# Performance work log

Hardware: AMD Instinct MI355X
Metric: run time of the kernel (lower is better)

Reference implementation:

```python
import jax, jax.numpy as jnp
import numpy as np

DIM = 20
N = 200000
E = 6400000
ITERATIONS = 3


def setup_inputs() -> dict:
    key = jax.random.key(0)
    ks = jax.random.split(key, 20)
    inp = {
        "h": jax.random.normal(ks[0], (N, DIM), dtype=jnp.float32),
        "node2depth": jax.random.randint(ks[1], (N,), 0, 5, dtype=jnp.int32),
        "edge_src": jax.random.randint(ks[2], (E,), 0, N, dtype=jnp.int32),
        "edge_dst": jax.random.randint(ks[3], (E,), 0, N, dtype=jnp.int32),
    }
    # Six DIM x DIM Linear layers (weight stored [out,in] like torch, plus bias)
    scale = 1.0 / np.sqrt(DIM)
    names = ["Wz", "Uz", "Wr", "Ur", "Wh", "Uh"]
    for j, nm in enumerate(names):
        inp[nm + "_w"] = jax.random.uniform(ks[4 + 2 * j], (DIM, DIM), jnp.float32, -scale, scale)
        inp[nm + "_b"] = jax.random.uniform(ks[5 + 2 * j], (DIM,), jnp.float32, -scale, scale)
    return inp


def _linear(x, w, b):
    return x @ w.T + b


def reference(h, Wz_w, Wz_b, Uz_w, Uz_b, Wr_w, Wr_b, Ur_w, Ur_b,
              Wh_w, Wh_b, Uh_w, Uh_b, node2depth, edge_src, edge_dst):
    active = None
    for i in range(ITERATIONS):
        # active set shrinks as i grows (depth + i <= ITERATIONS)
        active = (node2depth + i) <= ITERATIONS  # [N] bool
        af = active.astype(h.dtype)
        # x[u] = sum over neighbors v of h[v], counting only active src AND active dst
        msg = h[edge_src] * af[edge_src][:, None]          # [E, DIM]
        x = jax.ops.segment_sum(msg, edge_dst, num_segments=N)  # [N, DIM]
        x = x * af[:, None]
        z = jax.nn.sigmoid(_linear(x, Wz_w, Wz_b) + _linear(h, Uz_w, Uz_b))
        r = jax.nn.sigmoid(_linear(x, Wr_w, Wr_b) + _linear(h, Ur_w, Ur_b))
        h_cand = jnp.tanh(_linear(x, Wh_w, Wh_b) + _linear(r * h, Uh_w, Uh_b))
        h_new = z * h + (1.0 - z) * h_cand
        # inactive nodes are dropped from the dict in the original; since the
        # active set only shrinks, keeping their old h is equivalent
        h = jnp.where(active[:, None], h_new, h)
    # original returns only nodes active at the last iteration; zero out the rest
    return jnp.where(active[:, None], h, jnp.zeros_like(h))
```

## Files before the change

### kernel.cpp

```cpp
#include <hip/hip_runtime.h>

#define DIM    20
#define NN     200000
#define EE     6400000
#define ITERS  3
#define BLOCK  256

#define NODES_PER_FINE   64
#define NFINE            3125
#define NCOARSE          98
#define FINE_PER_COARSE  32

#define TILE1            2048
#define IPT1             8

#define TILE             4096
#define IPT              16

#define CAP1             57344
#define NT2P             14
#define CAP2             2048
#define PQ               2

typedef unsigned int u32;

__global__ void init_cursors(int* __restrict__ coarse_cursor,
                             int* __restrict__ fine_cursor,
                             int* __restrict__ gcur) {
    int g = blockIdx.x * 256 + threadIdx.x;
    if (g < NCOARSE) coarse_cursor[g] = g * CAP1;
    if (g < NFINE)   fine_cursor[g]   = g * CAP2;
    if (g == 0) *gcur = 0;
}

__global__ __launch_bounds__(BLOCK) void kdep(const int* __restrict__ depth,
                                              int* __restrict__ dcnt) {
    __shared__ u32 dh[5];
    int tid = threadIdx.x;
    if (tid < 5) dh[tid] = 0;
    __syncthreads();
    for (int n = blockIdx.x * BLOCK + tid; n < NN; n += gridDim.x * BLOCK)
        atomicAdd(&dh[depth[n]], 1u);
    __syncthreads();
    if (tid < 5) dcnt[tid * 256 + blockIdx.x] = (int)dh[tid];
}

__global__ __launch_bounds__(BLOCK) void k2_scan(const int* __restrict__ dcnt,
                                                 int* __restrict__ dbase,
                                                 int* __restrict__ cum) {
    __shared__ int wsum[4];
    __shared__ int sdb[1281];
    int tid = threadIdx.x;
    int lane = tid & 63, wid = tid >> 6;
    const int CH2 = 5;
    int loc[CH2];
    int base = tid * CH2;
    int s = 0;
    #pragma unroll
    for (int j = 0; j < CH2; ++j) { int v = dcnt[base + j]; loc[j] = v; s += v; }
    int incl = s;
    #pragma unroll
    for (int off = 1; off < 64; off <<= 1) {
        int t = __shfl_up(incl, off, 64);
        if (lane >= off) incl += t;
    }
    if (lane == 63) wsum[wid] = incl;
    __syncthreads();
    int woff = 0;
    for (int w = 0; w < wid; ++w) woff += wsum[w];
    int run = woff + incl - s;
    #pragma unroll
    for (int j = 0; j < CH2; ++j) {
        sdb[base + j]   = run;
        dbase[base + j] = run;
        run += loc[j];
    }
    if (tid == 255) sdb[1280] = run;
    __syncthreads();
    if (tid < 5) cum[tid] = sdb[(tid + 1) * 256];
}

__global__ __launch_bounds__(BLOCK) void kd_scatter(const int* __restrict__ depth,
                                                    const int* __restrict__ dbase,
                                                    int* __restrict__ perm) {
    __shared__ u32 dh[5];
    int tid = threadIdx.x;
    if (tid < 5) dh[tid] = 0;
    __syncthreads();
    for (int n = blockIdx.x * BLOCK + tid; n < NN; n += gridDim.x * BLOCK) {
        int d = depth[n];
        u32 r = atomicAdd(&dh[d], 1u);
        perm[n] = dbase[d * 256 + blockIdx.x] + (int)r;
    }
}

__global__ __launch_bounds__(BLOCK) void p1_split(const int* __restrict__ esrc,
                                                  const int* __restrict__ edst,
                                                  const int* __restrict__ perm,
                                                  const int* __restrict__ cum,
                                                  int* __restrict__ coarse_cursor,
                                                  u32* __restrict__ buf1) {
    __shared__ u32 hist[NCOARSE];
    __shared__ u32 lbase[NCOARSE];
    __shared__ u32 gbase[NCOARSE];
    __shared__ u32 lout[TILE1];
    int tid = threadIdx.x;
    int start = blockIdx.x * TILE1;
    if (tid < NCOARSE) hist[tid] = 0;
    __syncthreads();
    const u32 c3 = (u32)cum[3];

    int4 d4[2], s4[2];
    #pragma unroll
    for (int q = 0; q < 2; ++q) {
        int e4 = start + (q * BLOCK + tid) * 4;
        d4[q] = *(const int4*)(edst + e4);
        s4[q] = *(const int4*)(esrc + e4);
    }
    u32 pid[IPT1];
    pid[0] = (u32)perm[s4[0].x]; pid[1] = (u32)perm[s4[0].y];
    pid[2] = (u32)perm[s4[0].z]; pid[3] = (u32)perm[s4[0].w];
    pid[4] = (u32)perm[s4[1].x]; pid[5] = (u32)perm[s4[1].y];
    pid[6] = (u32)perm[s4[1].z]; pid[7] = (u32)perm[s4[1].w];
    asm volatile("" :: "v"(pid[0]), "v"(pid[1]), "v"(pid[2]), "v"(pid[3]),
                       "v"(pid[4]), "v"(pid[5]), "v"(pid[6]), "v"(pid[7]));
    int dd[IPT1];
    dd[0]=d4[0].x; dd[1]=d4[0].y; dd[2]=d4[0].z; dd[3]=d4[0].w;
    dd[4]=d4[1].x; dd[5]=d4[1].y; dd[6]=d4[1].z; dd[7]=d4[1].w;

    u32 rank[IPT1];
    #pragma unroll
    for (int k = 0; k < IPT1; ++k)
        if (pid[k] < c3) rank[k] = atomicAdd(&hist[(u32)dd[k] >> 11], 1u);
    __syncthreads();

    if (tid < 64) {
        u32 a = hist[tid];
        u32 b = (tid + 64 < NCOARSE) ? hist[tid + 64] : 0u;
        u32 ia = a, ib = b;
        #pragma unroll
        for (int off = 1; off < 64; off <<= 1) {
            u32 ta = (u32)__shfl_up((int)ia, off, 64);
            u32 tb = (u32)__shfl_up((int)ib, off, 64);
            if (tid >= off) { ia += ta; ib += tb; }
        }
        u32 totA = (u32)__shfl((int)ia, 63, 64);
        lbase[tid] = ia - a;
        if (tid + 64 < NCOARSE) lbase[tid + 64] = totA + ib - b;
    }
    __syncthreads();
    if (tid < NCOARSE) {
        u32 cq = hist[tid];
        gbase[tid] = cq ? (u32)atomicAdd((u32*)&coarse_cursor[tid], cq) : 0u;
    }
    #pragma unroll
    for (int k = 0; k < IPT1; ++k)
        if (pid[k] < c3)
            lout[lbase[(u32)dd[k] >> 11] + rank[k]] = ((u32)dd[k] & 2047u) | (pid[k] << 11);
    __syncthreads();
    int wid = tid >> 6, lane = tid & 63;
    for (int b = wid; b < NCOARSE; b += 4) {
        u32 cq = hist[b], lb = lbase[b], gb = gbase[b];
        for (u32 i = lane; i < cq; i += 64)
            buf1[gb + i] = lout[lb + i];
    }
}

__global__ __launch_bounds__(BLOCK) void p2_split(const u32* __restrict__ buf1,
                                                  const int* __restrict__ coarse_cursor,
                                                  int* __restrict__ fine_cursor,
                                                  u32* __restrict__ buf2) {
    int bid = blockIdx.x;
    int c = bid / NT2P, t = bid - c * NT2P;
    int base  = c * CAP1;
    int end   = coarse_cursor[c];
    int start = base + t * TILE;
    if (start >= end) return;

    __shared__ u32 hist[FINE_PER_COARSE];
    __shared__ u32 lbase[FINE_PER_COARSE];
    __shared__ u32 gbase[FINE_PER_COARSE];
    __shared__ u32 lout[TILE];
    int tid = threadIdx.x;
    if (tid < FINE_PER_COARSE) hist[tid] = 0;
    __syncthreads();

    u32 w[IPT];
    #pragma unroll
    for (int q = 0; q < 4; ++q) {
        int i4 = start + (q * BLOCK + tid) * 4;
        if (i4 + 3 < end) {
            uint4 v = *(const uint4*)(buf1 + i4);
            w[q * 4 + 0] = v.x; w[q * 4 + 1] = v.y;
            w[q * 4 + 2] = v.z; w[q * 4 + 3] = v.w;
        } else {
            #pragma unroll
            for (int j = 0; j < 4; ++j) {
                int i = i4 + j;
                w[q * 4 + j] = (i < end) ? buf1[i] : 0xFFFFFFFFu;
            }
        }
    }
    u32 rank[IPT];
    #pragma unroll
    for (int k = 0; k < IPT; ++k)
        if (w[k] != 0xFFFFFFFFu)
            rank[k] = atomicAdd(&hist[(w[k] & 2047u) >> 6], 1u);
    __syncthreads();

    if (tid < 32) {
        u32 a = hist[tid], ia = a;
        #pragma unroll
        for (int off = 1; off < 32; off <<= 1) {
            u32 ta = (u32)__shfl_up((int)ia, off, 32);
            if (tid >= off) ia += ta;
        }
        lbase[tid] = ia - a;
        int f = c * FINE_PER_COARSE + tid;
        gbase[tid] = a ? (u32)atomicAdd((u32*)&fine_cursor[f], a) : 0u;
    }
    __syncthreads();
    #pragma unroll
    for (int k = 0; k < IPT; ++k)
        if (w[k] != 0xFFFFFFFFu)
            lout[lbase[(w[k] & 2047u) >> 6] + rank[k]] = (w[k] & 63u) | ((w[k] >> 11) << 6);
    __syncthreads();
    int wid = tid >> 6, lane = tid & 63;
    for (int b = wid; b < FINE_PER_COARSE; b += 4) {
        u32 cq = hist[b], lb = lbase[b], gb = gbase[b];
        for (u32 i = lane; i < cq; i += 64)
            buf2[gb + i] = lout[lb + i];
    }
}

__global__ __launch_bounds__(BLOCK) void pb_sort(const u32* __restrict__ buf2,
                                                 const int* __restrict__ fine_cursor,
                                                 const int* __restrict__ cum,
                                                 int* __restrict__ gcur,
                                                 int* __restrict__ ptr,
                                                 u32* __restrict__ cnt3,
                                                 u32* __restrict__ ssrc) {
    __shared__ u32 hist[512];
    __shared__ u32 ebase[512];
    __shared__ u32 lout[CAP2];
    __shared__ u32 wsum[4];
    __shared__ int slo;
    int tid = threadIdx.x;
    int f = blockIdx.x;
    int base = f * CAP2;
    int end  = fine_cursor[f];
    int cnt  = end - base;
    u32 c0 = (u32)cum[0], c1 = (u32)cum[1], c2 = (u32)cum[2], c3 = (u32)cum[3];
    hist[tid] = 0; hist[tid + 256] = 0;
    __syncthreads();

    u32 w[PQ * 4];
    #pragma unroll
    for (int q = 0; q < PQ; ++q) {
        int i4 = base + (q * BLOCK + tid) * 4;
        if (i4 + 3 < end) {
            uint4 v = *(const uint4*)(buf2 + i4);
            w[q * 4 + 0] = v.x; w[q * 4 + 1] = v.y;
            w[q * 4 + 2] = v.z; w[q * 4 + 3] = v.w;
        } else {
            #pragma unroll
            for (int j = 0; j < 4; ++j) {
                int i = i4 + j;
                w[q * 4 + j] = (i < end) ? buf2[i] : 0xFFFFFFFFu;
            }
        }
    }
    u32 key[PQ * 4], rank[PQ * 4];
    #pragma unroll
    for (int k = 0; k < PQ * 4; ++k) {
        if (w[k] != 0xFFFFFFFFu) {
            u32 pid = w[k] >> 6;
            u32 dep = (u32)(pid >= c0) + (u32)(pid >= c1)
                    + (u32)(pid >= c2) + (u32)(pid >= c3);
            key[k]  = (w[k] & 63u) * 8u + dep;
            rank[k] = atomicAdd(&hist[key[k]], 1u);
        }
    }
    if (tid == 0) slo = atomicAdd(gcur, cnt);
    __syncthreads();
    {
        u32 s0 = hist[2 * tid], s1 = hist[2 * tid + 1];
        u32 s = s0 + s1;
        int lane = tid & 63, wid = tid >> 6;
        u32 incl = s;
        #pragma unroll
        for (int off = 1; off < 64; off <<= 1) {
            u32 t = __shfl_up((int)incl, off, 64);
            if (lane >= off) incl += t;
        }
        if (lane == 63) wsum[wid] = incl;
        __syncthreads();
        u32 woff = 0;
        for (int w2 = 0; w2 < wid; ++w2) woff += wsum[w2];
        u32 excl = woff + incl - s;
        ebase[2 * tid]     = excl;
        ebase[2 * tid + 1] = excl + s0;
    }
    __syncthreads();
    int lo = slo;
    if (tid < NODES_PER_FINE) {
        u32 base0 = ebase[tid * 8];
        u32 cc1 = ebase[tid * 8 + 2] - base0;
        u32 cc2 = ebase[tid * 8 + 3] - base0;
        u32 cc3 = ebase[tid * 8 + 4] - base0;
        int u = f * NODES_PER_FINE + tid;
        ptr[u]  = lo + (int)base0;
        cnt3[u] = cc1 | (cc2 << 10) | (cc3 << 20);
    }
    #pragma unroll
    for (int k = 0; k < PQ * 4; ++k) {
        if (w[k] != 0xFFFFFFFFu) lout[ebase[key[k]] + rank[k]] = w[k] >> 6;
    }
    __syncthreads();
    for (int j = tid; j < cnt; j += BLOCK) ssrc[lo + j] = lout[j];
}

__device__ __forceinline__ u32 pack_bf16x2(float a, float b) {
    u32 ua = __float_as_uint(a);
    u32 ub = __float_as_uint(b);
    ua = (ua + 0x7FFFu + ((ua >> 16) & 1u)) >> 16;
    ub = (ub + 0x7FFFu + ((ub >> 16) & 1u)) & 0xFFFF0000u;
    return ua | ub;
}

__global__ __launch_bounds__(BLOCK) void hconv(const float* __restrict__ h,
                                               u32* __restrict__ hbA,
                                               u32* __restrict__ hbC,
                                               const int* __restrict__ perm,
                                               const int* __restrict__ depth) {
    int g = blockIdx.x * BLOCK + threadIdx.x;
    if (g >= NN * 8) return;
    int node = g >> 3, s = g & 7;
    if (depth[node] > ITERS) return;
    int pid = perm[node];
    float2 f = *(const float2*)(h + (size_t)node * DIM + s * 2);
    hbA[(size_t)pid * 8 + s] = pack_bf16x2(f.x, f.y);
    if (s < 2) {
        float2 fc = *(const float2*)(h + (size_t)node * DIM + 16 + s * 2);
        hbC[(size_t)pid * 2 + s] = pack_bf16x2(fc.x, fc.y);
    }
}


__device__ __forceinline__ float bl(u32 w) { return __uint_as_float(w << 16); }
__device__ __forceinline__ float bh(u32 w) { return __uint_as_float(w & 0xFFFF0000u); }

__device__ __forceinline__ void acc_half(float* xa, float* xc, uint4 a, u32 c) {
    xa[0]+=bl(a.x); xa[1]+=bh(a.x);
    xa[2]+=bl(a.y); xa[3]+=bh(a.y);
    xa[4]+=bl(a.z); xa[5]+=bh(a.z);
    xa[6]+=bl(a.w); xa[7]+=bh(a.w);
    xc[0]+=bl(c);   xc[1]+=bh(c);
}

__global__ __launch_bounds__(BLOCK) void gather_x(
    const u32* __restrict__ hbA, const u32* __restrict__ hbC,
    const int* __restrict__ depth, const int* __restrict__ ptr,
    const u32* __restrict__ cnt3, const u32* __restrict__ ssrc,
    float* __restrict__ xg, int lim, int shift)
{
    int tid = threadIdx.x;
    int u = blockIdx.x * 32 + (tid >> 3);
    int j = tid & 7;
    int r = j >> 1;
    int q = j & 1;
    if (depth[u] > lim) return;
    int p = ptr[u];
    int d = (int)((cnt3[u] >> shift) & 1023u);

    float xa[8], xc[2];
    #pragma unroll
    for (int k = 0; k < 8; ++k) xa[k] = 0.0f;
    xc[0] = 0.0f; xc[1] = 0.0f;

    int e = r;
    for (; e + 12 < d; e += 16) {
        u32 p0 = ssrc[p + e];
        u32 p1 = ssrc[p + e + 4];
        u32 p2 = ssrc[p + e + 8];
        u32 p3 = ssrc[p + e + 12];
        uint4 a0 = *(const uint4*)(hbA + (size_t)p0 * 8 + q * 4);
        uint4 a1 = *(const uint4*)(hbA + (size_t)p1 * 8 + q * 4);
        uint4 a2 = *(const uint4*)(hbA + (size_t)p2 * 8 + q * 4);
        uint4 a3 = *(const uint4*)(hbA + (size_t)p3 * 8 + q * 4);
        u32 c0 = hbC[(size_t)p0 * 2 + q];
        u32 c1 = hbC[(size_t)p1 * 2 + q];
        u32 c2 = hbC[(size_t)p2 * 2 + q];
        u32 c3 = hbC[(size_t)p3 * 2 + q];
        acc_half(xa, xc, a0, c0);
        acc_half(xa, xc, a1, c1);
        acc_half(xa, xc, a2, c2);
        acc_half(xa, xc, a3, c3);
    }
    for (; e + 4 < d; e += 8) {
        u32 p0 = ssrc[p + e];
        u32 p1 = ssrc[p + e + 4];
        uint4 a0 = *(const uint4*)(hbA + (size_t)p0 * 8 + q * 4);
        uint4 a1 = *(const uint4*)(hbA + (size_t)p1 * 8 + q * 4);
        u32 c0 = hbC[(size_t)p0 * 2 + q];
        u32 c1 = hbC[(size_t)p1 * 2 + q];
        acc_half(xa, xc, a0, c0);
        acc_half(xa, xc, a1, c1);
    }
    if (e < d) {
        u32 p0 = ssrc[p + e];
        uint4 a0 = *(const uint4*)(hbA + (size_t)p0 * 8 + q * 4);
        u32 c0 = hbC[(size_t)p0 * 2 + q];
        acc_half(xa, xc, a0, c0);
    }
    #pragma unroll
    for (int k = 0; k < 8; ++k) {
        xa[k] += __shfl_xor(xa[k], 2, 64);
        xa[k] += __shfl_xor(xa[k], 4, 64);
    }
    xc[0] += __shfl_xor(xc[0], 2, 64); xc[0] += __shfl_xor(xc[0], 4, 64);
    xc[1] += __shfl_xor(xc[1], 2, 64); xc[1] += __shfl_xor(xc[1], 4, 64);

    float* xr = xg + (size_t)u * DIM;
    if (j == 0) {
        *(float4*)(xr)      = make_float4(xa[0], xa[1], xa[2], xa[3]);
        *(float4*)(xr + 4)  = make_float4(xa[4], xa[5], xa[6], xa[7]);
        *(float2*)(xr + 16) = make_float2(xc[0], xc[1]);
    } else if (j == 1) {
        *(float4*)(xr + 8)  = make_float4(xa[0], xa[1], xa[2], xa[3]);
        *(float4*)(xr + 12) = make_float4(xa[4], xa[5], xa[6], xa[7]);
        *(float2*)(xr + 18) = make_float2(xc[0], xc[1]);
    }
}


__device__ __forceinline__ float fast_sigmoid(float t) {
    return 1.0f / (1.0f + __expf(-t));
}
__device__ __forceinline__ float fast_tanh(float t) {
    t = fminf(fmaxf(t, -15.0f), 15.0f);
    float e2 = __expf(2.0f * t);
    return (e2 - 1.0f) / (e2 + 1.0f);
}

__global__ __launch_bounds__(BLOCK) void gru_update(
    const float* __restrict__ xg,
    const float* __restrict__ h_in, float* __restrict__ h_out,
    u32* __restrict__ hbA, u32* __restrict__ hbC,
    const int* __restrict__ depth, const int* __restrict__ perm,
    const int* __restrict__ cum,
    const float* __restrict__ Wz, const float* __restrict__ bWz,
    const float* __restrict__ Uz, const float* __restrict__ bUz,
    const float* __restrict__ Wr, const float* __restrict__ bWr,
    const float* __restrict__ Ur, const float* __restrict__ bUr,
    const float* __restrict__ Wh, const float* __restrict__ bWh,
    const float* __restrict__ Uh, const float* __restrict__ bUh,
    int lim, int cumIdx, int isFinal)
{
    int u = blockIdx.x * BLOCK + threadIdx.x;
    if (u >= NN) return;
    bool act = depth[u] <= lim;
    if (!act) {
        if (isFinal) {
            float4 z4 = make_float4(0.f, 0.f, 0.f, 0.f);
            float4* o4 = (float4*)(h_out + (size_t)u * DIM);
            #pragma unroll
            for (int q = 0; q < 5; ++q) o4[q] = z4;
        }
        return;
    }

    float x[DIM], h[DIM];
    {
        const float4* xv = (const float4*)(xg + (size_t)u * DIM);
        float4 a0 = xv[0], a1 = xv[1], a2 = xv[2], a3 = xv[3], a4 = xv[4];
        x[0]=a0.x; x[1]=a0.y; x[2]=a0.z; x[3]=a0.w;
        x[4]=a1.x; x[5]=a1.y; x[6]=a1.z; x[7]=a1.w;
        x[8]=a2.x; x[9]=a2.y; x[10]=a2.z; x[11]=a2.w;
        x[12]=a3.x; x[13]=a3.y; x[14]=a3.z; x[15]=a3.w;
        x[16]=a4.x; x[17]=a4.y; x[18]=a4.z; x[19]=a4.w;
    }
    {
        const float4* hv = (const float4*)(h_in + (size_t)u * DIM);
        float4 a0 = hv[0], a1 = hv[1], a2 = hv[2], a3 = hv[3], a4 = hv[4];
        h[0]=a0.x; h[1]=a0.y; h[2]=a0.z; h[3]=a0.w;
        h[4]=a1.x; h[5]=a1.y; h[6]=a1.z; h[7]=a1.w;
        h[8]=a2.x; h[9]=a2.y; h[10]=a2.z; h[11]=a2.w;
        h[12]=a3.x; h[13]=a3.y; h[14]=a3.z; h[15]=a3.w;
        h[16]=a4.x; h[17]=a4.y; h[18]=a4.z; h[19]=a4.w;
    }

    float z[DIM], rh[DIM];
    #pragma unroll
    for (int j = 0; j < DIM; ++j) {
        float sz = bWz[j] + bUz[j];
        float sr = bWr[j] + bUr[j];
        #pragma unroll
        for (int k = 0; k < DIM; ++k) {
            sz += x[k] * Wz[j * DIM + k];
            sz += h[k] * Uz[j * DIM + k];
            sr += x[k] * Wr[j * DIM + k];
            sr += h[k] * Ur[j * DIM + k];
        }
        z[j]  = fast_sigmoid(sz);
        rh[j] = fast_sigmoid(sr) * h[j];
    }

    float o[DIM];
    #pragma unroll
    for (int j = 0; j < DIM; ++j) {
        float sh = bWh[j] + bUh[j];
        #pragma unroll
        for (int k = 0; k < DIM; ++k) {
            sh += x[k]  * Wh[j * DIM + k];
            sh += rh[k] * Uh[j * DIM + k];
        }
        float hc = fast_tanh(sh);
        o[j] = z[j] * h[j] + (1.0f - z[j]) * hc;
    }

    {
        float4* o4 = (float4*)(h_out + (size_t)u * DIM);
        o4[0] = make_float4(o[0],  o[1],  o[2],  o[3]);
        o4[1] = make_float4(o[4],  o[5],  o[6],  o[7]);
        o4[2] = make_float4(o[8],  o[9],  o[10], o[11]);
        o4[3] = make_float4(o[12], o[13], o[14], o[15]);
        o4[4] = make_float4(o[16], o[17], o[18], o[19]);
    }
    if (!isFinal) {
        int pid = perm[u];
        if (pid < cum[cumIdx]) {
            u32* rowA = hbA + (size_t)pid * 8;
            uint4 wA0 = make_uint4(pack_bf16x2(o[0], o[1]),   pack_bf16x2(o[2], o[3]),
                                   pack_bf16x2(o[4], o[5]),   pack_bf16x2(o[6], o[7]));
            uint4 wA1 = make_uint4(pack_bf16x2(o[8], o[9]),   pack_bf16x2(o[10], o[11]),
                                   pack_bf16x2(o[12], o[13]), pack_bf16x2(o[14], o[15]));
            *(uint4*)rowA       = wA0;
            *(uint4*)(rowA + 4) = wA1;
            *(uint2*)(hbC + (size_t)pid * 2) =
                make_uint2(pack_bf16x2(o[16], o[17]), pack_bf16x2(o[18], o[19]));
        }
    }
}


extern "C" void kernel_launch(void* const* d_in, const int* in_sizes, int n_in,
                              void* d_out, int out_size, void* d_ws, size_t ws_size,
                              hipStream_t stream) {
    const float* h0    = (const float*)d_in[0];
    const int*   depth = (const int*)d_in[1];
    const int*   esrc  = (const int*)d_in[2];
    const int*   edst  = (const int*)d_in[3];
    const float* Wz  = (const float*)d_in[4];  const float* bWz = (const float*)d_in[5];
    const float* Uz  = (const float*)d_in[6];  const float* bUz = (const float*)d_in[7];
    const float* Wr  = (const float*)d_in[8];  const float* bWr = (const float*)d_in[9];
    const float* Ur  = (const float*)d_in[10]; const float* bUr = (const float*)d_in[11];
    const float* Wh  = (const float*)d_in[12]; const float* bWh = (const float*)d_in[13];
    const float* Uh  = (const float*)d_in[14]; const float* bUh = (const float*)d_in[15];
    float* out = (float*)d_out;

    int* W = (int*)d_ws;
    int*  dcnt          = W + 0;
    int*  dbase         = W + 1280;
    int*  cum           = W + 2560;
    int*  gcur          = W + 2568;
    int*  coarse_cursor = W + 2576;
    int*  fine_cursor   = W + 2688;
    int*  ptr           = W + 5824;
    u32*  cnt3          = (u32*)(W + 205824);
    int*  perm          = W + 405824;
    u32*  buf1          = (u32*)(W + 605824);
    u32*  buf2          = buf1 + (size_t)NCOARSE * CAP1;
    float* h1           = (float*)(buf2 + (size_t)NFINE * CAP2);
    u32*  hbA           = (u32*)(h1 + (size_t)NN * DIM);
    u32*  hbC           = hbA + (size_t)NN * 8;
    u32*  ssrc          = buf1;
    float* xg           = (float*)buf2;

    init_cursors<<<13, 256, 0, stream>>>(coarse_cursor, fine_cursor, gcur);
    kdep        <<<256, BLOCK, 0, stream>>>(depth, dcnt);
    k2_scan     <<<1,   BLOCK, 0, stream>>>(dcnt, dbase, cum);
    kd_scatter  <<<256, BLOCK, 0, stream>>>(depth, dbase, perm);
    p1_split    <<<EE / TILE1, BLOCK, 0, stream>>>(esrc, edst, perm, cum, coarse_cursor, buf1);
    p2_split    <<<NCOARSE * NT2P, BLOCK, 0, stream>>>(buf1, coarse_cursor, fine_cursor, buf2);
    pb_sort     <<<NFINE, BLOCK, 0, stream>>>(buf2, fine_cursor, cum, gcur, ptr, cnt3, ssrc);
    hconv       <<<(NN * 8) / BLOCK, BLOCK, 0, stream>>>(h0, hbA, hbC, perm, depth);

    gather_x  <<<NN / 32, BLOCK, 0, stream>>>(hbA, hbC, depth, ptr, cnt3, ssrc, xg, 3, 20);
    gru_update<<<(NN + BLOCK - 1) / BLOCK, BLOCK, 0, stream>>>(xg, h0, h1, hbA, hbC, depth, perm, cum,
        Wz, bWz, Uz, bUz, Wr, bWr, Ur, bUr, Wh, bWh, Uh, bUh, 3, 2, 0);
    gather_x  <<<NN / 32, BLOCK, 0, stream>>>(hbA, hbC, depth, ptr, cnt3, ssrc, xg, 2, 10);
    gru_update<<<(NN + BLOCK - 1) / BLOCK, BLOCK, 0, stream>>>(xg, h1, h1, hbA, hbC, depth, perm, cum,
        Wz, bWz, Uz, bUz, Wr, bWr, Ur, bUr, Wh, bWh, Uh, bUh, 2, 1, 0);
    gather_x  <<<NN / 32, BLOCK, 0, stream>>>(hbA, hbC, depth, ptr, cnt3, ssrc, xg, 1, 0);
    gru_update<<<(NN + BLOCK - 1) / BLOCK, BLOCK, 0, stream>>>(xg, h1, out, hbA, hbC, depth, perm, cum,
        Wz, bWz, Uz, bUz, Wr, bWr, Ur, bUr, Wh, bWh, Uh, bUh, 1, 0, 1);
}
```

Baseline: 524.0 us.

## Replace depth permutation with packed depth table and keep all edges in binning

Removes the three-kernel depth counting, scan and permutation pass. Edge sources are now stored by original node id rather than by permuted id. Inactive-source edges are no longer filtered during the coarse split, and pb_sort instead looks up each source's depth class in a 4-bit packed table. This drops the random perm gathers in p1_split along with several launches, but more edges flow through the binning passes, so bucket capacities are enlarged. hbA/hbC rows are now indexed by node id, so gather locality no longer benefits from depth-ordered packing.

```diff
diff --git a/kernel.cpp b/kernel.cpp
--- a/kernel.cpp
+++ b/kernel.cpp
@@ -17,10 +17,10 @@
 #define TILE             4096
 #define IPT              16
 
-#define CAP1             57344
-#define NT2P             14
-#define CAP2             2048
-#define PQ               2
+#define CAP1             67584
+#define NT2P             17
+#define CAP2             2304
+#define PIPT             9
 
 typedef unsigned int u32;
 
@@ -33,71 +33,21 @@
     if (g == 0) *gcur = 0;
 }
 
-__global__ __launch_bounds__(BLOCK) void kdep(const int* __restrict__ depth,
-                                              int* __restrict__ dcnt) {
-    __shared__ u32 dh[5];
-    int tid = threadIdx.x;
-    if (tid < 5) dh[tid] = 0;
-    __syncthreads();
-    for (int n = blockIdx.x * BLOCK + tid; n < NN; n += gridDim.x * BLOCK)
-        atomicAdd(&dh[depth[n]], 1u);
-    __syncthreads();
-    if (tid < 5) dcnt[tid * 256 + blockIdx.x] = (int)dh[tid];
-}
-
-__global__ __launch_bounds__(BLOCK) void k2_scan(const int* __restrict__ dcnt,
-                                                 int* __restrict__ dbase,
-                                                 int* __restrict__ cum) {
-    __shared__ int wsum[4];
-    __shared__ int sdb[1281];
-    int tid = threadIdx.x;
-    int lane = tid & 63, wid = tid >> 6;
-    const int CH2 = 5;
-    int loc[CH2];
-    int base = tid * CH2;
-    int s = 0;
-    #pragma unroll
-    for (int j = 0; j < CH2; ++j) { int v = dcnt[base + j]; loc[j] = v; s += v; }
-    int incl = s;
-    #pragma unroll
-    for (int off = 1; off < 64; off <<= 1) {
-        int t = __shfl_up(incl, off, 64);
-        if (lane >= off) incl += t;
-    }
-    if (lane == 63) wsum[wid] = incl;
-    __syncthreads();
-    int woff = 0;
-    for (int w = 0; w < wid; ++w) woff += wsum[w];
-    int run = woff + incl - s;
-    #pragma unroll
-    for (int j = 0; j < CH2; ++j) {
-        sdb[base + j]   = run;
-        dbase[base + j] = run;
-        run += loc[j];
-    }
-    if (tid == 255) sdb[1280] = run;
-    __syncthreads();
-    if (tid < 5) cum[tid] = sdb[(tid + 1) * 256];
-}
-
-__global__ __launch_bounds__(BLOCK) void kd_scatter(const int* __restrict__ depth,
-                                                    const int* __restrict__ dbase,
-                                                    int* __restrict__ perm) {
-    __shared__ u32 dh[5];
-    int tid = threadIdx.x;
-    if (tid < 5) dh[tid] = 0;
-    __syncthreads();
-    for (int n = blockIdx.x * BLOCK + tid; n < NN; n += gridDim.x * BLOCK) {
-        int d = depth[n];
-        u32 r = atomicAdd(&dh[d], 1u);
-        perm[n] = dbase[d * 256 + blockIdx.x] + (int)r;
-    }
+__global__ __launch_bounds__(BLOCK) void ctab_build(const int* __restrict__ depth,
+                                                    u32* __restrict__ CT) {
+    int i = blockIdx.x * BLOCK + threadIdx.x;
+    if (i >= NN / 8) return;
+    int4 a = *(const int4*)(depth + i * 8);
+    int4 b = *(const int4*)(depth + i * 8 + 4);
+    u32 w = ((u32)a.x & 7u)        | (((u32)a.y & 7u) << 4)
+          | (((u32)a.z & 7u) << 8) | (((u32)a.w & 7u) << 12)
+          | (((u32)b.x & 7u) << 16)| (((u32)b.y & 7u) << 20)
+          | (((u32)b.z & 7u) << 24)| (((u32)b.w & 7u) << 28);
+    CT[i] = w;
 }
 
 __global__ __launch_bounds__(BLOCK) void p1_split(const int* __restrict__ esrc,
                                                   const int* __restrict__ edst,
-                                                  const int* __restrict__ perm,
-                                                  const int* __restrict__ cum,
                                                   int* __restrict__ coarse_cursor,
                                                   u32* __restrict__ buf1) {
     __shared__ u32 hist[NCOARSE];
@@ -108,7 +58,6 @@
     int start = blockIdx.x * TILE1;
     if (tid < NCOARSE) hist[tid] = 0;
     __syncthreads();
-    const u32 c3 = (u32)cum[3];
 
     int4 d4[2], s4[2];
     #pragma unroll
@@ -117,21 +66,16 @@
         d4[q] = *(const int4*)(edst + e4);
         s4[q] = *(const int4*)(esrc + e4);
     }
-    u32 pid[IPT1];
-    pid[0] = (u32)perm[s4[0].x]; pid[1] = (u32)perm[s4[0].y];
-    pid[2] = (u32)perm[s4[0].z]; pid[3] = (u32)perm[s4[0].w];
-    pid[4] = (u32)perm[s4[1].x]; pid[5] = (u32)perm[s4[1].y];
-    pid[6] = (u32)perm[s4[1].z]; pid[7] = (u32)perm[s4[1].w];
-    asm volatile("" :: "v"(pid[0]), "v"(pid[1]), "v"(pid[2]), "v"(pid[3]),
-                       "v"(pid[4]), "v"(pid[5]), "v"(pid[6]), "v"(pid[7]));
-    int dd[IPT1];
+    int dd[IPT1], ss[IPT1];
     dd[0]=d4[0].x; dd[1]=d4[0].y; dd[2]=d4[0].z; dd[3]=d4[0].w;
     dd[4]=d4[1].x; dd[5]=d4[1].y; dd[6]=d4[1].z; dd[7]=d4[1].w;
+    ss[0]=s4[0].x; ss[1]=s4[0].y; ss[2]=s4[0].z; ss[3]=s4[0].w;
+    ss[4]=s4[1].x; ss[5]=s4[1].y; ss[6]=s4[1].z; ss[7]=s4[1].w;
 
     u32 rank[IPT1];
     #pragma unroll
     for (int k = 0; k < IPT1; ++k)
-        if (pid[k] < c3) rank[k] = atomicAdd(&hist[(u32)dd[k] >> 11], 1u);
+        rank[k] = atomicAdd(&hist[(u32)dd[k] >> 11], 1u);
     __syncthreads();
 
     if (tid < 64) {
@@ -155,8 +99,7 @@
     }
     #pragma unroll
     for (int k = 0; k < IPT1; ++k)
-        if (pid[k] < c3)
-            lout[lbase[(u32)dd[k] >> 11] + rank[k]] = ((u32)dd[k] & 2047u) | (pid[k] << 11);
+        lout[lbase[(u32)dd[k] >> 11] + rank[k]] = ((u32)dd[k] & 2047u) | ((u32)ss[k] << 11);
     __syncthreads();
     int wid = tid >> 6, lane = tid & 63;
     for (int b = wid; b < NCOARSE; b += 4) {
@@ -235,7 +178,7 @@
 
 __global__ __launch_bounds__(BLOCK) void pb_sort(const u32* __restrict__ buf2,
                                                  const int* __restrict__ fine_cursor,
-                                                 const int* __restrict__ cum,
+                                                 const u32* __restrict__ CT,
                                                  int* __restrict__ gcur,
                                                  int* __restrict__ ptr,
                                                  u32* __restrict__ cnt3,
@@ -250,13 +193,12 @@
     int base = f * CAP2;
     int end  = fine_cursor[f];
     int cnt  = end - base;
-    u32 c0 = (u32)cum[0], c1 = (u32)cum[1], c2 = (u32)cum[2], c3 = (u32)cum[3];
     hist[tid] = 0; hist[tid + 256] = 0;
     __syncthreads();
 
-    u32 w[PQ * 4];
-    #pragma unroll
-    for (int q = 0; q < PQ; ++q) {
+    u32 w[PIPT];
+    #pragma unroll
+    for (int q = 0; q < 2; ++q) {
         int i4 = base + (q * BLOCK + tid) * 4;
         if (i4 + 3 < end) {
             uint4 v = *(const uint4*)(buf2 + i4);
@@ -270,14 +212,22 @@
             }
         }
     }
-    u32 key[PQ * 4], rank[PQ * 4];
-    #pragma unroll
-    for (int k = 0; k < PQ * 4; ++k) {
+    {
+        int i = base + 2 * BLOCK * 4 + tid;
+        w[8] = (i < end) ? buf2[i] : 0xFFFFFFFFu;
+    }
+    u32 cls[PIPT];
+    #pragma unroll
+    for (int k = 0; k < PIPT; ++k) {
+        u32 s = w[k] >> 6;
+        if (s > (u32)(NN - 1)) s = (u32)(NN - 1);
+        cls[k] = (CT[s >> 3] >> ((s & 7u) << 2)) & 7u;
+    }
+    u32 key[PIPT], rank[PIPT];
+    #pragma unroll
+    for (int k = 0; k < PIPT; ++k) {
         if (w[k] != 0xFFFFFFFFu) {
-            u32 pid = w[k] >> 6;
-            u32 dep = (u32)(pid >= c0) + (u32)(pid >= c1)
-                    + (u32)(pid >= c2) + (u32)(pid >= c3);
-            key[k]  = (w[k] & 63u) * 8u + dep;
+            key[k]  = (w[k] & 63u) * 8u + cls[k];
             rank[k] = atomicAdd(&hist[key[k]], 1u);
         }
     }
@@ -313,7 +263,7 @@
         cnt3[u] = cc1 | (cc2 << 10) | (cc3 << 20);
     }
     #pragma unroll
-    for (int k = 0; k < PQ * 4; ++k) {
+    for (int k = 0; k < PIPT; ++k) {
         if (w[k] != 0xFFFFFFFFu) lout[ebase[key[k]] + rank[k]] = w[k] >> 6;
     }
     __syncthreads();
@@ -331,18 +281,16 @@
 __global__ __launch_bounds__(BLOCK) void hconv(const float* __restrict__ h,
                                                u32* __restrict__ hbA,
                                                u32* __restrict__ hbC,
-                                               const int* __restrict__ perm,
                                                const int* __restrict__ depth) {
     int g = blockIdx.x * BLOCK + threadIdx.x;
     if (g >= NN * 8) return;
     int node = g >> 3, s = g & 7;
     if (depth[node] > ITERS) return;
-    int pid = perm[node];
     float2 f = *(const float2*)(h + (size_t)node * DIM + s * 2);
-    hbA[(size_t)pid * 8 + s] = pack_bf16x2(f.x, f.y);
+    hbA[(size_t)node * 8 + s] = pack_bf16x2(f.x, f.y);
     if (s < 2) {
         float2 fc = *(const float2*)(h + (size_t)node * DIM + 16 + s * 2);
-        hbC[(size_t)pid * 2 + s] = pack_bf16x2(fc.x, fc.y);
+        hbC[(size_t)node * 2 + s] = pack_bf16x2(fc.x, fc.y);
     }
 }
 
@@ -447,19 +395,19 @@
     const float* __restrict__ xg,
     const float* __restrict__ h_in, float* __restrict__ h_out,
     u32* __restrict__ hbA, u32* __restrict__ hbC,
-    const int* __restrict__ depth, const int* __restrict__ perm,
-    const int* __restrict__ cum,
+    const int* __restrict__ depth,
     const float* __restrict__ Wz, const float* __restrict__ bWz,
     const float* __restrict__ Uz, const float* __restrict__ bUz,
     const float* __restrict__ Wr, const float* __restrict__ bWr,
     const float* __restrict__ Ur, const float* __restrict__ bUr,
     const float* __restrict__ Wh, const float* __restrict__ bWh,
     const float* __restrict__ Uh, const float* __restrict__ bUh,
-    int lim, int cumIdx, int isFinal)
+    int lim, int limNext, int isFinal)
 {
     int u = blockIdx.x * BLOCK + threadIdx.x;
     if (u >= NN) return;
-    bool act = depth[u] <= lim;
+    int du = depth[u];
+    bool act = du <= lim;
     if (!act) {
         if (isFinal) {
             float4 z4 = make_float4(0.f, 0.f, 0.f, 0.f);
@@ -527,19 +475,16 @@
         o4[3] = make_float4(o[12], o[13], o[14], o[15]);
         o4[4] = make_float4(o[16], o[17], o[18], o[19]);
     }
-    if (!isFinal) {
-        int pid = perm[u];
-        if (pid < cum[cumIdx]) {
-            u32* rowA = hbA + (size_t)pid * 8;
-            uint4 wA0 = make_uint4(pack_bf16x2(o[0], o[1]),   pack_bf16x2(o[2], o[3]),
-                                   pack_bf16x2(o[4], o[5]),   pack_bf16x2(o[6], o[7]));
-            uint4 wA1 = make_uint4(pack_bf16x2(o[8], o[9]),   pack_bf16x2(o[10], o[11]),
-                                   pack_bf16x2(o[12], o[13]), pack_bf16x2(o[14], o[15]));
-            *(uint4*)rowA       = wA0;
-            *(uint4*)(rowA + 4) = wA1;
-            *(uint2*)(hbC + (size_t)pid * 2) =
-                make_uint2(pack_bf16x2(o[16], o[17]), pack_bf16x2(o[18], o[19]));
-        }
+    if (!isFinal && du <= limNext) {
+        u32* rowA = hbA + (size_t)u * 8;
+        uint4 wA0 = make_uint4(pack_bf16x2(o[0], o[1]),   pack_bf16x2(o[2], o[3]),
+                               pack_bf16x2(o[4], o[5]),   pack_bf16x2(o[6], o[7]));
+        uint4 wA1 = make_uint4(pack_bf16x2(o[8], o[9]),   pack_bf16x2(o[10], o[11]),
+                               pack_bf16x2(o[12], o[13]), pack_bf16x2(o[14], o[15]));
+        *(uint4*)rowA       = wA0;
+        *(uint4*)(rowA + 4) = wA1;
+        *(uint2*)(hbC + (size_t)u * 2) =
+            make_uint2(pack_bf16x2(o[16], o[17]), pack_bf16x2(o[18], o[19]));
     }
 }
 
@@ -560,16 +505,13 @@
     float* out = (float*)d_out;
 
     int* W = (int*)d_ws;
-    int*  dcnt          = W + 0;
-    int*  dbase         = W + 1280;
-    int*  cum           = W + 2560;
-    int*  gcur          = W + 2568;
-    int*  coarse_cursor = W + 2576;
-    int*  fine_cursor   = W + 2688;
-    int*  ptr           = W + 5824;
-    u32*  cnt3          = (u32*)(W + 205824);
-    int*  perm          = W + 405824;
-    u32*  buf1          = (u32*)(W + 605824);
+    u32*  CT            = (u32*)(W + 0);
+    int*  gcur          = W + 25024;
+    int*  coarse_cursor = W + 25088;
+    int*  fine_cursor   = W + 25216;
+    int*  ptr           = W + 28416;
+    u32*  cnt3          = (u32*)(W + 228416);
+    u32*  buf1          = (u32*)(W + 428416);
     u32*  buf2          = buf1 + (size_t)NCOARSE * CAP1;
     float* h1           = (float*)(buf2 + (size_t)NFINE * CAP2);
     u32*  hbA           = (u32*)(h1 + (size_t)NN * DIM);
@@ -578,21 +520,19 @@
     float* xg           = (float*)buf2;
 
     init_cursors<<<13, 256, 0, stream>>>(coarse_cursor, fine_cursor, gcur);
-    kdep        <<<256, BLOCK, 0, stream>>>(depth, dcnt);
-    k2_scan     <<<1,   BLOCK, 0, stream>>>(dcnt, dbase, cum);
-    kd_scatter  <<<256, BLOCK, 0, stream>>>(depth, dbase, perm);
-    p1_split    <<<EE / TILE1, BLOCK, 0, stream>>>(esrc, edst, perm, cum, coarse_cursor, buf1);
+    ctab_build  <<<(NN / 8 + BLOCK - 1) / BLOCK, BLOCK, 0, stream>>>(depth, CT);
+    p1_split    <<<EE / TILE1, BLOCK, 0, stream>>>(esrc, edst, coarse_cursor, buf1);
     p2_split    <<<NCOARSE * NT2P, BLOCK, 0, stream>>>(buf1, coarse_cursor, fine_cursor, buf2);
-    pb_sort     <<<NFINE, BLOCK, 0, stream>>>(buf2, fine_cursor, cum, gcur, ptr, cnt3, ssrc);
-    hconv       <<<(NN * 8) / BLOCK, BLOCK, 0, stream>>>(h0, hbA, hbC, perm, depth);
+    pb_sort     <<<NFINE, BLOCK, 0, stream>>>(buf2, fine_cursor, CT, gcur, ptr, cnt3, ssrc);
+    hconv       <<<(NN * 8) / BLOCK, BLOCK, 0, stream>>>(h0, hbA, hbC, depth);
 
     gather_x  <<<NN / 32, BLOCK, 0, stream>>>(hbA, hbC, depth, ptr, cnt3, ssrc, xg, 3, 20);
-    gru_update<<<(NN + BLOCK - 1) / BLOCK, BLOCK, 0, stream>>>(xg, h0, h1, hbA, hbC, depth, perm, cum,
+    gru_update<<<(NN + BLOCK - 1) / BLOCK, BLOCK, 0, stream>>>(xg, h0, h1, hbA, hbC, depth,
         Wz, bWz, Uz, bUz, Wr, bWr, Ur, bUr, Wh, bWh, Uh, bUh, 3, 2, 0);
     gather_x  <<<NN / 32, BLOCK, 0, stream>>>(hbA, hbC, depth, ptr, cnt3, ssrc, xg, 2, 10);
-    gru_update<<<(NN + BLOCK - 1) / BLOCK, BLOCK, 0, stream>>>(xg, h1, h1, hbA, hbC, depth, perm, cum,
+    gru_update<<<(NN + BLOCK - 1) / BLOCK, BLOCK, 0, stream>>>(xg, h1, h1, hbA, hbC, depth,
         Wz, bWz, Uz, bUz, Wr, bWr, Ur, bUr, Wh, bWh, Uh, bUh, 2, 1, 0);
     gather_x  <<<NN / 32, BLOCK, 0, stream>>>(hbA, hbC, depth, ptr, cnt3, ssrc, xg, 1, 0);
-    gru_update<<<(NN + BLOCK - 1) / BLOCK, BLOCK, 0, stream>>>(xg, h1, out, hbA, hbC, depth, perm, cum,
+    gru_update<<<(NN + BLOCK - 1) / BLOCK, BLOCK, 0, stream>>>(xg, h1, out, hbA, hbC, depth,
         Wz, bWz, Uz, bUz, Wr, bWr, Ur, bUr, Wh, bWh, Uh, bUh, 1, 0, 1);
 }
```

Result: no change. 530.3 us (+1.2%).
